# Kernel tuning notes

Measured on AMD Instinct MI355X. Metric: run time of the kernel, lower is better.

## Reference

```python
import jax, jax.numpy as jnp
import numpy as np

AUDIO_DIM, SEM_DIM, ATTN_DIM = 512, 768, 128


def setup_inputs() -> dict:
    key = jax.random.key(0)
    ks = jax.random.split(key, 12)
    B, T, T_sem = 8, 4096, 1024
    s = lambda d: 1.0 / np.sqrt(d)
    return {
        "x_ct": jax.random.normal(ks[0], (B, AUDIO_DIM, T), jnp.float32),
        "sem_btd": jax.random.normal(ks[1], (B, T_sem, SEM_DIM), jnp.float32),
        "ln_w": jnp.ones((AUDIO_DIM,), jnp.float32),
        "ln_b": jnp.zeros((AUDIO_DIM,), jnp.float32),
        "Wq": jax.random.normal(ks[2], (AUDIO_DIM, ATTN_DIM), jnp.float32) * s(AUDIO_DIM),
        "bq": jnp.zeros((ATTN_DIM,), jnp.float32),
        "Wk": jax.random.normal(ks[3], (SEM_DIM, ATTN_DIM), jnp.float32) * s(SEM_DIM),
        "bk": jnp.zeros((ATTN_DIM,), jnp.float32),
        "Wv": jax.random.normal(ks[4], (SEM_DIM, ATTN_DIM), jnp.float32) * s(SEM_DIM),
        "bv": jnp.zeros((ATTN_DIM,), jnp.float32),
        "Wo": jax.random.normal(ks[5], (ATTN_DIM, AUDIO_DIM), jnp.float32) * s(ATTN_DIM),
        "bo": jnp.zeros((AUDIO_DIM,), jnp.float32),
    }


def _layernorm(x, w, b, eps=1e-5):
    mu = jnp.mean(x, axis=-1, keepdims=True)
    var = jnp.mean(jnp.square(x - mu), axis=-1, keepdims=True)
    return (x - mu) * jax.lax.rsqrt(var + eps) * w + b


def reference(x_ct, sem_btd, ln_w, ln_b, Wq, bq, Wk, bk, Wv, bv, Wo, bo):
    # x_ct: [B, C, T] -> [B, T, C]
    x = jnp.swapaxes(x_ct, 1, 2)
    x = _layernorm(x, ln_w, ln_b)
    Q = x @ Wq + bq                      # [B, T, A]
    K = sem_btd @ Wk + bk                # [B, S, A]
    V = sem_btd @ Wv + bv                # [B, S, A]
    scale = ATTN_DIM ** -0.5
    attn = jnp.einsum("bta,bsa->bts", Q, K) * scale
    attn = jax.nn.softmax(attn, axis=-1)  # dropout: eval mode (identity)
    ctx = jnp.einsum("bts,bsa->bta", attn, V)
    delta = ctx @ Wo + bo                # [B, T, C]
    return jnp.swapaxes(delta, 1, 2)     # [B, C, T]
```

## Files before the change

### kernel.cpp

```cpp
#include <hip/hip_runtime.h>
#include <hip/hip_bf16.h>
#include <math.h>

#define BATCH 8
#define TDIM 4096
#define SDIM 1024
#define CDIM 512
#define DDIM 768
#define ADIM 128

typedef short s8v __attribute__((ext_vector_type(8)));
typedef float f4v __attribute__((ext_vector_type(4)));

__device__ __forceinline__ short f2bf(float f) {
    unsigned u = __float_as_uint(f);
    u += 0x7fffu + ((u >> 16) & 1u);
    return (short)(u >> 16);
}
__device__ __forceinline__ float bf2f(short s) {
    return __uint_as_float(((unsigned)(unsigned short)s) << 16);
}
__device__ __forceinline__ f4v mfma16(s8v a, s8v b, f4v c) {
    return __builtin_amdgcn_mfma_f32_16x16x32_bf16(a, b, c, 0, 0, 0);
}

__global__ __launch_bounds__(256) void prep_w(
    const float* __restrict__ Wq, const float* __restrict__ Wk,
    const float* __restrict__ Wv, const float* __restrict__ Wo,
    short* __restrict__ WqT, short* __restrict__ WkT,
    short* __restrict__ WvT, short* __restrict__ WoT)
{
    int gid = blockIdx.x * 256 + threadIdx.x;
    {
        int k = gid >> 7, n = gid & 127;
        WqT[n * 512 + k] = f2bf(Wq[gid]);
    }
    #pragma unroll
    for (int i = 0; i < 2; ++i) {
        int e = gid + i * 65536;
        if (e < 98304) {
            int k = e >> 7, n = e & 127;
            WkT[n * 768 + k] = f2bf(Wk[e]);
            WvT[n * 768 + k] = f2bf(Wv[e]);
        }
    }
    {
        int k = gid >> 9, c = gid & 511;
        WoT[c * 128 + k] = f2bf(Wo[gid]);
    }
}

__global__ __launch_bounds__(256) void kv_proj(
    const float* __restrict__ sem,
    const short* __restrict__ WkT, const float* __restrict__ bk,
    const short* __restrict__ WvT, const float* __restrict__ bv,
    short* __restrict__ Kb, short* __restrict__ Vb)
{
    __shared__ __align__(16) short sA[32 * 40];
    __shared__ __align__(16) short sW[2][128 * 40];
    const int tid = threadIdx.x, lane = tid & 63, wave = tid >> 6;
    const int ln15 = lane & 15, q = lane >> 4, kq = q * 8;
    const int r0 = blockIdx.x * 32;
    const int b = r0 >> 10, sbase = r0 & 1023;
    const int kv = wave >> 1;
    const int mh = wave & 1;
    const int m  = mh * 16 + ln15;

    f4v acc[8];
    #pragma unroll
    for (int j = 0; j < 8; ++j) acc[j] = (f4v)0.0f;

    const int srow = tid >> 3;
    const int sk4  = (tid & 7) * 4;

    for (int kc = 0; kc < DDIM / 32; ++kc) {
        __syncthreads();
        {
            float4 f = *(const float4*)&sem[(size_t)(r0 + srow) * DDIM + kc * 32 + sk4];
            uint2 pk;
            pk.x = (unsigned short)f2bf(f.x) | ((unsigned)(unsigned short)f2bf(f.y) << 16);
            pk.y = (unsigned short)f2bf(f.z) | ((unsigned)(unsigned short)f2bf(f.w) << 16);
            *(uint2*)&sA[srow * 40 + sk4] = pk;
        }
        #pragma unroll
        for (int i = 0; i < 2; ++i) {
            int idx8 = i * 256 + tid;
            int n = idx8 >> 2, k8 = (idx8 & 3) * 8;
            *(s8v*)&sW[0][n * 40 + k8] = *(const s8v*)&WkT[(size_t)n * 768 + kc * 32 + k8];
            *(s8v*)&sW[1][n * 40 + k8] = *(const s8v*)&WvT[(size_t)n * 768 + kc * 32 + k8];
        }
        __syncthreads();
        s8v a = *(const s8v*)&sA[m * 40 + kq];
        #pragma unroll
        for (int j = 0; j < 8; ++j) {
            s8v bb = *(const s8v*)&sW[kv][(j * 16 + ln15) * 40 + kq];
            acc[j] = mfma16(a, bb, acc[j]);
        }
    }
    const int s_in_b = sbase + mh * 16 + q * 4;
    if (kv == 0) {
        #pragma unroll
        for (int j = 0; j < 8; ++j) {
            int col = j * 16 + ln15;
            float bias = bk[col];
            #pragma unroll
            for (int r = 0; r < 4; ++r)
                Kb[((size_t)b * SDIM + s_in_b + r) * ADIM + col] = f2bf(acc[j][r] + bias);
        }
    } else {
        #pragma unroll
        for (int j = 0; j < 8; ++j) {
            int col = j * 16 + ln15;
            float bias = bv[col];
            uint2 pk;
            pk.x = (unsigned short)f2bf(acc[j][0] + bias) | ((unsigned)(unsigned short)f2bf(acc[j][1] + bias) << 16);
            pk.y = (unsigned short)f2bf(acc[j][2] + bias) | ((unsigned)(unsigned short)f2bf(acc[j][3] + bias) << 16);
            *(uint2*)&Vb[((size_t)b * ADIM + col) * SDIM + s_in_b] = pk;
        }
    }
}

__global__ __launch_bounds__(256) void ln_q(
    const float* __restrict__ x, const float* __restrict__ lnw, const float* __restrict__ lnb,
    const short* __restrict__ WqT, const float* __restrict__ bq, short* __restrict__ Qb)
{
    __shared__ __align__(16) short xt[32 * 512];
    __shared__ __align__(16) char  ubuf[128 * 72 * 2];
    __shared__ float smu[32], srs[32];
    short* sWq  = (short*)ubuf;
    float* red1 = (float*)ubuf;
    float* red2 = (float*)(ubuf + 4224);
    const int tid = threadIdx.x, lane = tid & 63, wave = tid >> 6;
    const int ln15 = lane & 15, q = lane >> 4, kq = q * 8;
    const int b = blockIdx.x >> 7;
    const int t0 = (blockIdx.x & 127) * 32;
    const float* xb = x + (size_t)b * CDIM * TDIM;

    const int tq = (tid & 7) * 4;
    const int g  = tid >> 3;
    float ps1[4] = {0.f,0.f,0.f,0.f}, ps2[4] = {0.f,0.f,0.f,0.f};
    #pragma unroll
    for (int i = 0; i < 16; ++i) {
        int c = i * 32 + g;
        float4 f = *(const float4*)&xb[(size_t)c * TDIM + t0 + tq];
        float vv[4] = { f.x, f.y, f.z, f.w };
        int kb = c >> 3, cl = c & 7;
        #pragma unroll
        for (int jj = 0; jj < 4; ++jj) {
            int t = tq + jj;
            ps1[jj] += vv[jj]; ps2[jj] += vv[jj] * vv[jj];
            xt[t * 512 + ((kb ^ ((t >> 2) & 7)) * 8) + cl] = f2bf(vv[jj]);
        }
    }
    #pragma unroll
    for (int jj = 0; jj < 4; ++jj) {
        red1[(tq + jj) * 33 + g] = ps1[jj];
        red2[(tq + jj) * 33 + g] = ps2[jj];
    }
    __syncthreads();
    if (tid < 32) {
        float s1 = 0.f, s2 = 0.f;
        #pragma unroll 8
        for (int gg = 0; gg < 32; ++gg) { s1 += red1[tid * 33 + gg]; s2 += red2[tid * 33 + gg]; }
        float mu = s1 * (1.f / 512.f);
        float var = s2 * (1.f / 512.f) - mu * mu;
        smu[tid] = mu; srs[tid] = rsqrtf(var + 1e-5f);
    }
    __syncthreads();
    {
        const int cb = tid & 63;
        const int c8 = cb * 8;
        float w8[8], b8[8];
        #pragma unroll
        for (int jj = 0; jj < 8; ++jj) { w8[jj] = lnw[c8 + jj]; b8[jj] = lnb[c8 + jj]; }
        #pragma unroll
        for (int i = 0; i < 8; ++i) {
            int t = i * 4 + (tid >> 6);
            float mu = smu[t], rs = srs[t];
            short* p = &xt[t * 512 + ((cb ^ ((t >> 2) & 7)) * 8)];
            s8v v = *(s8v*)p;
            #pragma unroll
            for (int jj = 0; jj < 8; ++jj)
                v[jj] = f2bf((bf2f(v[jj]) - mu) * rs * w8[jj] + b8[jj]);
            *(s8v*)p = v;
        }
    }
    f4v acc[4];
    #pragma unroll
    for (int j = 0; j < 4; ++j) acc[j] = (f4v)0.0f;
    const int mrow = (wave & 1) * 16 + ln15;
    const int jb = (wave >> 1) * 4;
    for (int kc = 0; kc < 8; ++kc) {
        __syncthreads();
        #pragma unroll
        for (int i = 0; i < 4; ++i) {
            int idx8 = i * 256 + tid;
            int n = idx8 >> 3, k8 = (idx8 & 7) * 8;
            *(s8v*)&sWq[n * 72 + k8] = *(const s8v*)&WqT[(size_t)n * 512 + kc * 64 + k8];
        }
        __syncthreads();
        #pragma unroll
        for (int kk = 0; kk < 2; ++kk) {
            int kb = kc * 8 + kk * 4 + q;
            s8v a = *(const s8v*)&xt[mrow * 512 + ((kb ^ ((mrow >> 2) & 7)) * 8)];
            #pragma unroll
            for (int j = 0; j < 4; ++j) {
                s8v bb = *(const s8v*)&sWq[((jb + j) * 16 + ln15) * 72 + kk * 32 + kq];
                acc[j] = mfma16(a, bb, acc[j]);
            }
        }
    }
    const float scale = 0.08838834764831845f;
    #pragma unroll
    for (int j = 0; j < 4; ++j) {
        int col = (jb + j) * 16 + ln15;
        float bias = bq[col];
        #pragma unroll
        for (int r = 0; r < 4; ++r) {
            int t = t0 + (wave & 1) * 16 + q * 4 + r;
            Qb[((size_t)b * TDIM + t) * ADIM + col] = f2bf((acc[j][r] + bias) * scale);
        }
    }
}

__global__ __launch_bounds__(256) void attn(
    const short* __restrict__ Qb, const short* __restrict__ Kb,
    const short* __restrict__ Vb, short* __restrict__ Cx)
{
    __shared__ __align__(16) short sK [2][64 * 128];
    __shared__ __align__(16) short sVT[2][128 * 64];
    __shared__ __align__(16) short sP [64 * 64];
    const int tid = threadIdx.x, lane = tid & 63, wave = tid >> 6;
    const int ln15 = lane & 15, q = lane >> 4, kq = q * 8;
    const int b = blockIdx.x >> 6;
    const int t0 = (blockIdx.x & 63) * 64;
    const int m = wave * 16 + ln15;

    const int krow = tid >> 4, kkb = tid & 15;
    const int varow = tid >> 3, vkb = tid & 7;

    s8v qf[4];
    {
        const short* qp = Qb + ((size_t)b * TDIM + t0 + m) * ADIM + kq;
        #pragma unroll
        for (int kc = 0; kc < 4; ++kc) qf[kc] = *(const s8v*)(qp + kc * 32);
    }
    s8v ones;
    #pragma unroll
    for (int j = 0; j < 8; ++j) ones[j] = (short)0x3F80;

    f4v accO[8]; f4v accL = (f4v)0.0f;
    #pragma unroll
    for (int j = 0; j < 8; ++j) accO[j] = (f4v)0.0f;

    const short* Kbase = Kb + (size_t)b * SDIM * ADIM;
    const short* Vbase = Vb + (size_t)b * ADIM * SDIM;
    s8v rk[4], rv[4];

    #pragma unroll
    for (int i = 0; i < 4; ++i) {
        rk[i] = *(const s8v*)(Kbase + (size_t)(i * 16 + krow) * ADIM + kkb * 8);
        rv[i] = *(const s8v*)(Vbase + (size_t)(i * 32 + varow) * SDIM + vkb * 8);
    }
    #pragma unroll
    for (int i = 0; i < 4; ++i) {
        int r = i * 16 + krow;
        *(s8v*)&sK[0][r * 128 + ((kkb ^ (r & 15)) * 8)] = rk[i];
        int a = i * 32 + varow;
        *(s8v*)&sVT[0][a * 64 + ((vkb ^ (a & 7)) * 8)] = rv[i];
    }
    __syncthreads();

    for (int sc = 0; sc < SDIM / 64; ++sc) {
        const int cur = sc & 1;
        if (sc < 15) {
            const int s0n = (sc + 1) * 64;
            #pragma unroll
            for (int i = 0; i < 4; ++i) {
                rk[i] = *(const s8v*)(Kbase + (size_t)(s0n + i * 16 + krow) * ADIM + kkb * 8);
                rv[i] = *(const s8v*)(Vbase + (size_t)(i * 32 + varow) * SDIM + s0n + vkb * 8);
            }
        }
        #pragma unroll
        for (int j = 0; j < 4; ++j) {
            f4v sacc = (f4v)0.0f;
            const int row = j * 16 + ln15;
            #pragma unroll
            for (int kc = 0; kc < 4; ++kc) {
                s8v bb = *(const s8v*)&sK[cur][row * 128 + (((kc * 4 + q) ^ (row & 15)) * 8)];
                sacc = mfma16(qf[kc], bb, sacc);
            }
            #pragma unroll
            for (int r = 0; r < 4; ++r) {
                float ev = __expf(sacc[r]);
                int prow = wave * 16 + q * 4 + r;
                int pcol = j * 16 + ln15;
                sP[prow * 64 + (((pcol >> 3) ^ (prow & 7)) * 8) + (pcol & 7)] = f2bf(ev);
            }
        }
        #pragma unroll
        for (int kc = 0; kc < 2; ++kc) {
            s8v pa = *(const s8v*)&sP[m * 64 + (((kc * 4 + q) ^ (m & 7)) * 8)];
            accL = mfma16(pa, ones, accL);
            #pragma unroll
            for (int j = 0; j < 8; ++j) {
                int a = j * 16 + ln15;
                s8v bb = *(const s8v*)&sVT[cur][a * 64 + (((kc * 4 + q) ^ (a & 7)) * 8)];
                accO[j] = mfma16(pa, bb, accO[j]);
            }
        }
        if (sc < 15) {
            #pragma unroll
            for (int i = 0; i < 4; ++i) {
                int r = i * 16 + krow;
                *(s8v*)&sK[cur ^ 1][r * 128 + ((kkb ^ (r & 15)) * 8)] = rk[i];
                int a = i * 32 + varow;
                *(s8v*)&sVT[cur ^ 1][a * 64 + ((vkb ^ (a & 7)) * 8)] = rv[i];
            }
        }
        __syncthreads();
    }
    #pragma unroll
    for (int r = 0; r < 4; ++r) {
        float rinv = 1.0f / accL[r];
        int t = t0 + wave * 16 + q * 4 + r;
        #pragma unroll
        for (int j = 0; j < 8; ++j) {
            int col = j * 16 + ln15;
            Cx[((size_t)b * TDIM + t) * ADIM + col] = f2bf(accO[j][r] * rinv);
        }
    }
}

__global__ __launch_bounds__(256) void out_proj(
    const short* __restrict__ Cx, const short* __restrict__ WoT,
    const float* __restrict__ bo, float* __restrict__ out)
{
    __shared__ __align__(16) short sCtx[64 * 136];
    __shared__ __align__(16) char  buf[128 * 136 * 2];
    short* sWoT = (short*)buf;
    float* outT = (float*)buf;
    const int tid = threadIdx.x, lane = tid & 63, wave = tid >> 6;
    const int ln15 = lane & 15, q = lane >> 4, kq = q * 8;
    const int b = blockIdx.x >> 8;
    const int rem = blockIdx.x & 255;
    const int t0 = (rem & 63) * 64;
    const int c0 = (rem >> 6) * 128;

    #pragma unroll
    for (int i = 0; i < 4; ++i) {
        int idx8 = i * 256 + tid;
        int row = idx8 >> 4, a8 = (idx8 & 15) * 8;
        *(s8v*)&sCtx[row * 136 + a8] = *(const s8v*)&Cx[((size_t)b * TDIM + t0 + row) * ADIM + a8];
    }
    #pragma unroll
    for (int i = 0; i < 8; ++i) {
        int idx8 = i * 256 + tid;
        int n = idx8 >> 4, k8 = (idx8 & 15) * 8;
        *(s8v*)&sWoT[n * 136 + k8] = *(const s8v*)&WoT[(size_t)(c0 + n) * ADIM + k8];
    }
    __syncthreads();
    f4v acc[8];
    #pragma unroll
    for (int j = 0; j < 8; ++j) acc[j] = (f4v)0.0f;
    const int m = wave * 16 + ln15;
    #pragma unroll
    for (int kc = 0; kc < 4; ++kc) {
        s8v a = *(const s8v*)&sCtx[m * 136 + kc * 32 + kq];
        #pragma unroll
        for (int j = 0; j < 8; ++j) {
            s8v bb = *(const s8v*)&sWoT[(j * 16 + ln15) * 136 + kc * 32 + kq];
            acc[j] = mfma16(a, bb, acc[j]);
        }
    }
    __syncthreads();
    #pragma unroll
    for (int j = 0; j < 8; ++j) {
        int cl = j * 16 + ln15;
        float bias = bo[c0 + cl];
        #pragma unroll
        for (int r = 0; r < 4; ++r) {
            int tl = wave * 16 + q * 4 + r;
            outT[cl * 68 + tl] = acc[j][r] + bias;
        }
    }
    __syncthreads();
    #pragma unroll
    for (int i = 0; i < 8; ++i) {
        int idx4 = i * 256 + tid;
        int c = idx4 >> 4, t4 = (idx4 & 15) * 4;
        float4 v = *(const float4*)&outT[c * 68 + t4];
        *(float4*)&out[((size_t)b * CDIM + c0 + c) * TDIM + t0 + t4] = v;
    }
}

extern "C" void kernel_launch(void* const* d_in, const int* in_sizes, int n_in,
                              void* d_out, int out_size, void* d_ws, size_t ws_size,
                              hipStream_t stream) {
    const float* x   = (const float*)d_in[0];
    const float* sem = (const float*)d_in[1];
    const float* lnw = (const float*)d_in[2];
    const float* lnb = (const float*)d_in[3];
    const float* Wq  = (const float*)d_in[4];
    const float* bq  = (const float*)d_in[5];
    const float* Wk  = (const float*)d_in[6];
    const float* bk  = (const float*)d_in[7];
    const float* Wv  = (const float*)d_in[8];
    const float* bv  = (const float*)d_in[9];
    const float* Wo  = (const float*)d_in[10];
    const float* bo  = (const float*)d_in[11];
    float* out = (float*)d_out;

    short* ws  = (short*)d_ws;
    short* Qb  = ws;
    short* Kb  = Qb  + (size_t)BATCH * TDIM * ADIM;
    short* Vb  = Kb  + (size_t)BATCH * SDIM * ADIM;
    short* Cx  = Vb  + (size_t)BATCH * SDIM * ADIM;
    short* WqT = Cx  + (size_t)BATCH * TDIM * ADIM;
    short* WkT = WqT + 128 * 512;
    short* WvT = WkT + 128 * 768;
    short* WoT = WvT + 128 * 768;

    hipLaunchKernelGGL(prep_w,  dim3(256),  dim3(256), 0, stream, Wq, Wk, Wv, Wo, WqT, WkT, WvT, WoT);
    hipLaunchKernelGGL(kv_proj, dim3(256),  dim3(256), 0, stream, sem, WkT, bk, WvT, bv, Kb, Vb);
    hipLaunchKernelGGL(ln_q,    dim3(1024), dim3(256), 0, stream, x, lnw, lnb, WqT, bq, Qb);
    hipLaunchKernelGGL(attn,    dim3(512),  dim3(256), 0, stream, Qb, Kb, Vb, Cx);
    hipLaunchKernelGGL(out_proj,dim3(2048), dim3(256), 0, stream, Cx, WoT, bo, out);
}
```

Measured before the change: 232.0 us.

## Fold LayerNorm affine into Wq and apply normalization after the Q GEMM

The LayerNorm weight is folded into the bf16 Wq during weight prep, and per-column sums u = sum(lnw*Wq) and v = sum(lnb*Wq)+bq are precomputed. The Q epilogue then computes rs*(acc - mu*u) + v, so the in-shared-memory normalization pass over the raw bf16 tile is dropped. The change also replaces the shared-memory stat reduction with wave shuffles, loads Wq fragments straight from global memory with register double buffering instead of staging them through LDS, widens the xt swizzle, and adds an occupancy hint. The GEMM now runs on un-centered bf16 inputs, which can lose precision when the input mean is large relative to its spread.

```diff
diff --git a/kernel.cpp b/kernel.cpp
--- a/kernel.cpp
+++ b/kernel.cpp
@@ -27,13 +27,17 @@
 __global__ __launch_bounds__(256) void prep_w(
     const float* __restrict__ Wq, const float* __restrict__ Wk,
     const float* __restrict__ Wv, const float* __restrict__ Wo,
+    const float* __restrict__ lnw, const float* __restrict__ lnb,
+    const float* __restrict__ bq,
     short* __restrict__ WqT, short* __restrict__ WkT,
-    short* __restrict__ WvT, short* __restrict__ WoT)
+    short* __restrict__ WvT, short* __restrict__ WoT,
+    float* __restrict__ uq, float* __restrict__ vq)
 {
+    __shared__ float su[2][128], sv[2][128];
     int gid = blockIdx.x * 256 + threadIdx.x;
     {
         int k = gid >> 7, n = gid & 127;
-        WqT[n * 512 + k] = f2bf(Wq[gid]);
+        WqT[n * 512 + k] = f2bf(Wq[gid] * lnw[k]);
     }
     #pragma unroll
     for (int i = 0; i < 2; ++i) {
@@ -47,6 +51,22 @@
     {
         int k = gid >> 9, c = gid & 511;
         WoT[c * 128 + k] = f2bf(Wo[gid]);
+    }
+    if (blockIdx.x == 255) {
+        int a = threadIdx.x & 127, half = threadIdx.x >> 7;
+        float s1 = 0.f, s2 = 0.f;
+        #pragma unroll 8
+        for (int c = half * 256; c < half * 256 + 256; ++c) {
+            float wv = Wq[c * 128 + a];
+            s1 += bf2f(f2bf(lnw[c] * wv));
+            s2 += lnb[c] * wv;
+        }
+        su[half][a] = s1; sv[half][a] = s2;
+        __syncthreads();
+        if (threadIdx.x < 128) {
+            uq[a] = su[0][a] + su[1][a];
+            vq[a] = sv[0][a] + sv[1][a] + bq[a];
+        }
     }
 }
 
@@ -120,16 +140,13 @@
     }
 }
 
-__global__ __launch_bounds__(256) void ln_q(
-    const float* __restrict__ x, const float* __restrict__ lnw, const float* __restrict__ lnb,
-    const short* __restrict__ WqT, const float* __restrict__ bq, short* __restrict__ Qb)
+__global__ __launch_bounds__(256, 4) void ln_q(
+    const float* __restrict__ x,
+    const short* __restrict__ WqT, const float* __restrict__ uq,
+    const float* __restrict__ vq, short* __restrict__ Qb)
 {
     __shared__ __align__(16) short xt[32 * 512];
-    __shared__ __align__(16) char  ubuf[128 * 72 * 2];
-    __shared__ float smu[32], srs[32];
-    short* sWq  = (short*)ubuf;
-    float* red1 = (float*)ubuf;
-    float* red2 = (float*)(ubuf + 4224);
+    __shared__ __align__(16) float redw[4][32][2];
     const int tid = threadIdx.x, lane = tid & 63, wave = tid >> 6;
     const int ln15 = lane & 15, q = lane >> 4, kq = q * 8;
     const int b = blockIdx.x >> 7;
@@ -149,76 +166,75 @@
         for (int jj = 0; jj < 4; ++jj) {
             int t = tq + jj;
             ps1[jj] += vv[jj]; ps2[jj] += vv[jj] * vv[jj];
-            xt[t * 512 + ((kb ^ ((t >> 2) & 7)) * 8) + cl] = f2bf(vv[jj]);
-        }
-    }
-    #pragma unroll
-    for (int jj = 0; jj < 4; ++jj) {
-        red1[(tq + jj) * 33 + g] = ps1[jj];
-        red2[(tq + jj) * 33 + g] = ps2[jj];
+            int swz = ((t >> 2) & 7) | ((t & 3) << 3);
+            xt[t * 512 + ((kb ^ swz) * 8) + cl] = f2bf(vv[jj]);
+        }
+    }
+    #pragma unroll
+    for (int mk = 8; mk <= 32; mk <<= 1) {
+        #pragma unroll
+        for (int jj = 0; jj < 4; ++jj) {
+            ps1[jj] += __shfl_xor(ps1[jj], mk, 64);
+            ps2[jj] += __shfl_xor(ps2[jj], mk, 64);
+        }
+    }
+    if ((lane >> 3) == 0) {
+        #pragma unroll
+        for (int jj = 0; jj < 4; ++jj) {
+            redw[wave][tq + jj][0] = ps1[jj];
+            redw[wave][tq + jj][1] = ps2[jj];
+        }
     }
     __syncthreads();
-    if (tid < 32) {
+
+    const int mrow = (wave & 1) * 16 + ln15;
+    const int jb = (wave >> 1) * 4;
+    const int swzm = ((mrow >> 2) & 7) | ((mrow & 3) << 3);
+    f4v acc[4];
+    #pragma unroll
+    for (int j = 0; j < 4; ++j) acc[j] = (f4v)0.0f;
+    s8v bbuf[2][4];
+    #pragma unroll
+    for (int j = 0; j < 4; ++j)
+        bbuf[0][j] = *(const s8v*)&WqT[(size_t)((jb + j) * 16 + ln15) * 512 + kq];
+    #pragma unroll
+    for (int kf = 0; kf < 16; ++kf) {
+        const int cur = kf & 1;
+        if (kf < 15) {
+            #pragma unroll
+            for (int j = 0; j < 4; ++j)
+                bbuf[cur ^ 1][j] = *(const s8v*)&WqT[(size_t)((jb + j) * 16 + ln15) * 512 + (kf + 1) * 32 + kq];
+        }
+        s8v a = *(const s8v*)&xt[mrow * 512 + (((kf * 4 + q) ^ swzm) * 8)];
+        #pragma unroll
+        for (int j = 0; j < 4; ++j)
+            acc[j] = mfma16(a, bbuf[cur][j], acc[j]);
+    }
+
+    float u4[4], v4[4];
+    #pragma unroll
+    for (int j = 0; j < 4; ++j) {
+        int col = (jb + j) * 16 + ln15;
+        u4[j] = uq[col]; v4[j] = vq[col];
+    }
+    const float scale = 0.08838834764831845f;
+    #pragma unroll
+    for (int r = 0; r < 4; ++r) {
+        int tl = (wave & 1) * 16 + q * 4 + r;
         float s1 = 0.f, s2 = 0.f;
-        #pragma unroll 8
-        for (int gg = 0; gg < 32; ++gg) { s1 += red1[tid * 33 + gg]; s2 += red2[tid * 33 + gg]; }
+        #pragma unroll
+        for (int w = 0; w < 4; ++w) {
+            float2 p = *(const float2*)&redw[w][tl][0];
+            s1 += p.x; s2 += p.y;
+        }
         float mu = s1 * (1.f / 512.f);
         float var = s2 * (1.f / 512.f) - mu * mu;
-        smu[tid] = mu; srs[tid] = rsqrtf(var + 1e-5f);
-    }
-    __syncthreads();
-    {
-        const int cb = tid & 63;
-        const int c8 = cb * 8;
-        float w8[8], b8[8];
-        #pragma unroll
-        for (int jj = 0; jj < 8; ++jj) { w8[jj] = lnw[c8 + jj]; b8[jj] = lnb[c8 + jj]; }
-        #pragma unroll
-        for (int i = 0; i < 8; ++i) {
-            int t = i * 4 + (tid >> 6);
-            float mu = smu[t], rs = srs[t];
-            short* p = &xt[t * 512 + ((cb ^ ((t >> 2) & 7)) * 8)];
-            s8v v = *(s8v*)p;
-            #pragma unroll
-            for (int jj = 0; jj < 8; ++jj)
-                v[jj] = f2bf((bf2f(v[jj]) - mu) * rs * w8[jj] + b8[jj]);
-            *(s8v*)p = v;
-        }
-    }
-    f4v acc[4];
-    #pragma unroll
-    for (int j = 0; j < 4; ++j) acc[j] = (f4v)0.0f;
-    const int mrow = (wave & 1) * 16 + ln15;
-    const int jb = (wave >> 1) * 4;
-    for (int kc = 0; kc < 8; ++kc) {
-        __syncthreads();
-        #pragma unroll
-        for (int i = 0; i < 4; ++i) {
-            int idx8 = i * 256 + tid;
-            int n = idx8 >> 3, k8 = (idx8 & 7) * 8;
-            *(s8v*)&sWq[n * 72 + k8] = *(const s8v*)&WqT[(size_t)n * 512 + kc * 64 + k8];
-        }
-        __syncthreads();
-        #pragma unroll
-        for (int kk = 0; kk < 2; ++kk) {
-            int kb = kc * 8 + kk * 4 + q;
-            s8v a = *(const s8v*)&xt[mrow * 512 + ((kb ^ ((mrow >> 2) & 7)) * 8)];
-            #pragma unroll
-            for (int j = 0; j < 4; ++j) {
-                s8v bb = *(const s8v*)&sWq[((jb + j) * 16 + ln15) * 72 + kk * 32 + kq];
-                acc[j] = mfma16(a, bb, acc[j]);
-            }
-        }
-    }
-    const float scale = 0.08838834764831845f;
-    #pragma unroll
-    for (int j = 0; j < 4; ++j) {
-        int col = (jb + j) * 16 + ln15;
-        float bias = bq[col];
-        #pragma unroll
-        for (int r = 0; r < 4; ++r) {
-            int t = t0 + (wave & 1) * 16 + q * 4 + r;
-            Qb[((size_t)b * TDIM + t) * ADIM + col] = f2bf((acc[j][r] + bias) * scale);
+        float rs = rsqrtf(var + 1e-5f);
+        int t = t0 + tl;
+        #pragma unroll
+        for (int j = 0; j < 4; ++j) {
+            float qv = (rs * (acc[j][r] - mu * u4[j]) + v4[j]) * scale;
+            Qb[((size_t)b * TDIM + t) * ADIM + ((jb + j) * 16 + ln15)] = f2bf(qv);
         }
     }
 }
@@ -420,10 +436,13 @@
     short* WkT = WqT + 128 * 512;
     short* WvT = WkT + 128 * 768;
     short* WoT = WvT + 128 * 768;
-
-    hipLaunchKernelGGL(prep_w,  dim3(256),  dim3(256), 0, stream, Wq, Wk, Wv, Wo, WqT, WkT, WvT, WoT);
+    float* uq  = (float*)(WoT + 512 * 128);
+    float* vq  = uq + 128;
+
+    hipLaunchKernelGGL(prep_w,  dim3(256),  dim3(256), 0, stream,
+                       Wq, Wk, Wv, Wo, lnw, lnb, bq, WqT, WkT, WvT, WoT, uq, vq);
     hipLaunchKernelGGL(kv_proj, dim3(256),  dim3(256), 0, stream, sem, WkT, bk, WvT, bv, Kb, Vb);
-    hipLaunchKernelGGL(ln_q,    dim3(1024), dim3(256), 0, stream, x, lnw, lnb, WqT, bq, Qb);
+    hipLaunchKernelGGL(ln_q,    dim3(1024), dim3(256), 0, stream, x, WqT, uq, vq, Qb);
     hipLaunchKernelGGL(attn,    dim3(512),  dim3(256), 0, stream, Qb, Kb, Vb, Cx);
     hipLaunchKernelGGL(out_proj,dim3(2048), dim3(256), 0, stream, Cx, WoT, bo, out);
 }
```

After: 264.4 us. 13.9% more time.
